# Performance work log

Measured on AMD Instinct MI355X. Metric: run time of the kernel, lower is better.

The kernel has to match this reference:

```python
import jax, jax.numpy as jnp
import numpy as np

EMBED = 1024
HEADS = 16
HDIM = EMBED // HEADS
B, S = 4, 2048
NEG = -1e20


def setup_inputs() -> dict:
    key = jax.random.key(0)
    ks = jax.random.split(key, 9)
    query = jax.random.normal(ks[0], (B, S, EMBED), dtype=jnp.float32)
    key_t = jax.random.normal(ks[1], (B, S, EMBED), dtype=jnp.float32)
    value = jax.random.normal(ks[2], (B, S, EMBED), dtype=jnp.float32)
    mask = jax.random.randint(ks[3], (1, 1, S, S), 0, 2, dtype=jnp.int32)
    padding = jax.random.randint(ks[4], (B, 1, 1, S), 0, 2, dtype=jnp.int32)
    sc = 1.0 / np.sqrt(EMBED)
    Wq = jax.random.normal(ks[5], (EMBED, EMBED), dtype=jnp.float32) * sc
    Wk = jax.random.normal(ks[6], (EMBED, EMBED), dtype=jnp.float32) * sc
    Wv = jax.random.normal(ks[7], (EMBED, EMBED), dtype=jnp.float32) * sc
    Wo = jax.random.normal(ks[8], (EMBED, EMBED), dtype=jnp.float32) * sc
    return {"query": query, "key": key_t, "value": value, "mask": mask,
            "padding": padding, "Wq": Wq, "Wk": Wk, "Wv": Wv, "Wo": Wo}


def reference(query, key, value, mask, padding, Wq, Wk, Wv, Wo):
    b, q_len, _ = query.shape
    k_len = key.shape[1]
    # projections (nn.Linear: x @ W^T), split into heads
    qs = (query @ Wq.T).reshape(b, q_len, HEADS, HDIM)
    ks = (key @ Wk.T).reshape(b, k_len, HEADS, HDIM)
    vs = (value @ Wv.T).reshape(b, k_len, HEADS, HDIM)
    scale = EMBED ** 0.25
    qs = qs / scale
    ks = ks / scale
    # [b, h, q, k] scores
    dot = jnp.einsum('bkhd,bqhd->bhqk', ks, qs)
    dot = jnp.where(mask == 0, NEG, dot)
    dot = jnp.where(padding == 0, NEG, dot)
    attn = jax.nn.softmax(dot, axis=-1)
    alpha = jnp.einsum('bhqk,bkhd->bqhd', attn, vs)
    out = alpha.reshape(b, q_len, EMBED) @ Wo.T
    return out
```

## Files before the change

kernel.cpp:

```cpp
#include <hip/hip_runtime.h>
#include <stdint.h>

#define B_  4
#define S_  2048
#define E_  1024
#define H_  16
#define D_  64

typedef __bf16 bf16;
typedef __bf16 bf16x4 __attribute__((ext_vector_type(4)));
typedef __bf16 bf16x8 __attribute__((ext_vector_type(8)));
typedef float  f32x4 __attribute__((ext_vector_type(4)));
typedef float  f32x16 __attribute__((ext_vector_type(16)));
typedef uint32_t u32x4 __attribute__((ext_vector_type(4)));

__device__ __forceinline__ f32x4 mfma16(bf16x8 a, bf16x8 b, f32x4 c) {
  return __builtin_amdgcn_mfma_f32_16x16x32_bf16(a, b, c, 0, 0, 0);
}
__device__ __forceinline__ f32x16 mfma32(bf16x8 a, bf16x8 b, f32x16 c) {
  return __builtin_amdgcn_mfma_f32_32x32x16_bf16(a, b, c, 0, 0, 0);
}

__device__ __forceinline__ int sw(int row, int idx) { return idx ^ ((row & 7) << 3); }

__device__ __forceinline__ void gl_lds16(const void* g, void* l) {
  __builtin_amdgcn_global_load_lds(
      (const __attribute__((address_space(1))) void*)g,
      (__attribute__((address_space(3))) void*)l, 16, 0, 0);
}

__device__ __forceinline__ uint32_t cvtpk(float lo, float hi) {
  uint32_t r;
  asm("v_cvt_pk_bf16_f32 %0, %1, %2" : "=v"(r) : "v"(lo), "v"(hi));
  return r;
}
__device__ __forceinline__ void plswap(uint32_t& a, uint32_t& b) {
  asm("v_permlane32_swap_b32 %0, %1" : "+v"(a), "+v"(b));
}

__global__ void pack_mask_kernel(const int* __restrict__ mask, uint32_t* __restrict__ mbits) {
  int idx = blockIdx.x * 256 + threadIdx.x;
  int q = idx >> 6, w = idx & 63;
  const int* p = mask + q * S_ + w * 32;
  uint32_t bits = 0;
#pragma unroll
  for (int j = 0; j < 32; j += 4) {
    int4 v = *(const int4*)(p + j);
    bits |= (v.x != 0 ? 1u : 0u) << (j + 0);
    bits |= (v.y != 0 ? 1u : 0u) << (j + 1);
    bits |= (v.z != 0 ? 1u : 0u) << (j + 2);
    bits |= (v.w != 0 ? 1u : 0u) << (j + 3);
  }
  mbits[idx] = bits;
}

__global__ void pack_pad_kernel(const int* __restrict__ pad, uint32_t* __restrict__ pbits) {
  int idx = threadIdx.x;
  int b = idx >> 6, w = idx & 63;
  const int* p = pad + b * S_ + w * 32;
  uint32_t bits = 0;
#pragma unroll
  for (int j = 0; j < 32; j += 4) {
    int4 v = *(const int4*)(p + j);
    bits |= (v.x != 0 ? 1u : 0u) << (j + 0);
    bits |= (v.y != 0 ? 1u : 0u) << (j + 1);
    bits |= (v.z != 0 ? 1u : 0u) << (j + 2);
    bits |= (v.w != 0 ? 1u : 0u) << (j + 3);
  }
  pbits[idx] = bits;
}

__global__ __launch_bounds__(256)
void cvt_act(const float* __restrict__ q, const float* __restrict__ k,
             const float* __restrict__ v, bf16* __restrict__ out) {
  const float* src = blockIdx.z == 0 ? q : (blockIdx.z == 1 ? k : v);
  size_t i = ((size_t)blockIdx.x * 256 + threadIdx.x) * 8;
  float4 a = *(const float4*)(src + i);
  float4 b = *(const float4*)(src + i + 4);
  bf16x8 o;
  o[0] = (bf16)a.x; o[1] = (bf16)a.y; o[2] = (bf16)a.z; o[3] = (bf16)a.w;
  o[4] = (bf16)b.x; o[5] = (bf16)b.y; o[6] = (bf16)b.z; o[7] = (bf16)b.w;
  *(bf16x8*)(out + (size_t)blockIdx.z * (8192ull * 1024ull) + i) = o;
}

__global__ __launch_bounds__(256)
void cvt_w(const float* __restrict__ w0, const float* __restrict__ w1,
           const float* __restrict__ w2, const float* __restrict__ w3,
           bf16* __restrict__ out, float sq, float sk) {
  int z = blockIdx.z;
  const float* src = z == 0 ? w0 : (z == 1 ? w1 : (z == 2 ? w2 : w3));
  float s = (z == 0) ? sq : ((z == 1) ? sk : 1.0f);
  size_t i = ((size_t)blockIdx.x * 256 + threadIdx.x) * 8;
  float4 a = *(const float4*)(src + i);
  float4 b = *(const float4*)(src + i + 4);
  bf16x8 o;
  o[0] = (bf16)(a.x * s); o[1] = (bf16)(a.y * s); o[2] = (bf16)(a.z * s); o[3] = (bf16)(a.w * s);
  o[4] = (bf16)(b.x * s); o[5] = (bf16)(b.y * s); o[6] = (bf16)(b.z * s); o[7] = (bf16)(b.w * s);
  *(bf16x8*)(out + (size_t)z * (1024ull * 1024ull) + i) = o;
}

struct GA { const bf16* A; const bf16* W; void* O; };

template<bool OUT_F32>
__global__ __launch_bounds__(256, 2)
void gemm_bf(GA g0, GA g1, GA g2) {
  GA g = (blockIdx.z == 0) ? g0 : ((blockIdx.z == 1) ? g1 : g2);
  const int tid = threadIdx.x;
  const int l = tid & 63, wv = tid >> 6;
  const int lg = l >> 4, lr = l & 15;
  const int wr = wv >> 1, wc = wv & 1;
  const int brow = blockIdx.x * 128, bcol = blockIdx.y * 128;
  const int sr = l >> 3, sc8 = l & 7;

  __shared__ bf16 As[128 * 64];
  __shared__ bf16 Bs[128 * 64];

  f32x4 acc[4][4] = {};

  const bf16* Ab = g.A + (size_t)(brow + wv * 32 + sr) * E_ + (size_t)(sc8 ^ sr) * 8;
  const bf16* Bb = g.W + (size_t)(bcol + wv * 32 + sr) * E_ + (size_t)(sc8 ^ sr) * 8;
  bf16* la = As + (wv * 32) * 64;
  bf16* lb = Bs + (wv * 32) * 64;

  for (int kt = 0; kt < E_ / 64; ++kt) {
    __syncthreads();
    const bf16* a = Ab + kt * 64;
    const bf16* b = Bb + kt * 64;
#pragma unroll
    for (int i = 0; i < 4; ++i) {
      gl_lds16(a + (size_t)i * 8 * E_, la + i * 8 * 64);
      gl_lds16(b + (size_t)i * 8 * E_, lb + i * 8 * 64);
    }
    __syncthreads();
#pragma unroll
    for (int kk = 0; kk < 2; ++kk) {
      bf16x8 af[4], bfr[4];
#pragma unroll
      for (int ms = 0; ms < 4; ++ms) {
        int row = wr * 64 + ms * 16 + lr;
        af[ms] = *(const bf16x8*)&As[sw(row, row * 64 + kk * 32 + lg * 8)];
      }
#pragma unroll
      for (int ns = 0; ns < 4; ++ns) {
        int row = wc * 64 + ns * 16 + lr;
        bfr[ns] = *(const bf16x8*)&Bs[sw(row, row * 64 + kk * 32 + lg * 8)];
      }
#pragma unroll
      for (int ms = 0; ms < 4; ++ms)
#pragma unroll
        for (int ns = 0; ns < 4; ++ns)
          acc[ms][ns] = mfma16(af[ms], bfr[ns], acc[ms][ns]);
    }
  }
#pragma unroll
  for (int ms = 0; ms < 4; ++ms) {
#pragma unroll
    for (int ns = 0; ns < 4; ++ns) {
#pragma unroll
      for (int r = 0; r < 4; ++r) {
        int row = brow + wr * 64 + ms * 16 + lg * 4 + r;
        int col = bcol + wc * 64 + ns * 16 + lr;
        if constexpr (OUT_F32) ((float*)g.O)[(size_t)row * E_ + col] = acc[ms][ns][r];
        else                   ((bf16*)g.O)[(size_t)row * E_ + col] = (bf16)acc[ms][ns][r];
      }
    }
  }
}

__global__ __launch_bounds__(256, 2)
void transpose_v(const bf16* __restrict__ V, bf16* __restrict__ Vt) {
  int bh = blockIdx.y; int b = bh >> 4, h = bh & 15;
  int s0 = blockIdx.x * 64;
  int tid = threadIdx.x;
  __shared__ bf16 t[64][72];
  int rb = tid >> 3, seg = tid & 7;
#pragma unroll
  for (int i = 0; i < 2; ++i) {
    int row = rb + 32 * i;
    bf16x8 v = *(const bf16x8*)(V + (size_t)(b * S_ + s0 + row) * E_ + h * 64 + seg * 8);
#pragma unroll
    for (int j = 0; j < 8; ++j) t[row][seg * 8 + j] = v[j];
  }
  __syncthreads();
#pragma unroll
  for (int i = 0; i < 2; ++i) {
    int d = rb + 32 * i;
    bf16x8 v;
#pragma unroll
    for (int j = 0; j < 8; ++j) v[j] = t[seg * 8 + j][d];
    *(bf16x8*)(Vt + ((size_t)bh * 64 + d) * S_ + s0 + seg * 8) = v;
  }
}

__global__ __launch_bounds__(256, 2)
void attn_kernel(const bf16* __restrict__ Q, const bf16* __restrict__ K,
                 const bf16* __restrict__ Vt, const uint32_t* __restrict__ mbits,
                 const uint32_t* __restrict__ pbits, bf16* __restrict__ alpha) {
  const int raw = blockIdx.x;
  const int xcd = raw & 7, slot = raw >> 3;
  const int bh = xcd * 8 + (slot >> 3), qblk = slot & 7;
  const int b = bh >> 4, h = bh & 15;
  const int tid = threadIdx.x, wv = tid >> 6, l = tid & 63;
  const int ln = l & 31, hi = l >> 5;
  const int qw = qblk * 256 + wv * 64;
  const int sr = l >> 3, sc8 = l & 7;
  const int g = (ln & 7) ^ (ln >> 3);

  __shared__ bf16 Ks[2][64 * 64];
  __shared__ bf16 Vs[2][64 * 64];

  bf16x8 qreg[2][4];
#pragma unroll
  for (int qt = 0; qt < 2; ++qt)
#pragma unroll
    for (int dc = 0; dc < 4; ++dc)
      qreg[qt][dc] = *(const bf16x8*)(Q + (size_t)(b * S_ + qw + qt * 32 + ln) * E_
                                        + h * 64 + dc * 16 + hi * 8);

  bf16x8 ones;
#pragma unroll
  for (int j = 0; j < 8; ++j) ones[j] = (bf16)1.0f;

  f32x16 o[2][2] = {};
  f32x16 lacc[2] = {};

  const bf16* Kb = K + (size_t)b * S_ * E_ + (size_t)h * 64;
  const bf16* Vb = Vt + (size_t)bh * 64 * S_;

  auto stage = [&](int buf, int kt) {
#pragma unroll
    for (int op = 0; op < 2; ++op) {
      int rb = wv * 16 + op * 8;
      int cK = (sc8 ^ sr ^ ((rb >> 3) & 7)) * 8;
      gl_lds16(Kb + (size_t)(kt * 64 + rb + sr) * E_ + cK, Ks[buf] + rb * 64);
      gl_lds16(Vb + (size_t)(rb + sr) * S_ + kt * 64 + cK, Vs[buf] + rb * 64);
    }
  };

  stage(0, 0);
  __syncthreads();

  for (int kt = 0; kt < S_ / 64; ++kt) {
    const int cur = kt & 1;
    if (kt + 1 < S_ / 64) stage(cur ^ 1, kt + 1);

    f32x16 sc[2][2] = {};
    __builtin_amdgcn_s_setprio(1);
#pragma unroll
    for (int ct = 0; ct < 2; ++ct) {
#pragma unroll
      for (int dc = 0; dc < 4; ++dc) {
        int row = ct * 32 + ln;
        int c = (dc * 2 + hi) ^ g ^ (ct * 4);
        bf16x8 kf = *(const bf16x8*)&Ks[cur][row * 64 + c * 8];
#pragma unroll
        for (int qt = 0; qt < 2; ++qt)
          sc[ct][qt] = mfma32(kf, qreg[qt][dc], sc[ct][qt]);
      }
    }
    __builtin_amdgcn_s_setprio(0);

    uint32_t pw0 = pbits[b * 64 + kt * 2], pw1 = pbits[b * 64 + kt * 2 + 1];
    uint32_t mq[2][2];
#pragma unroll
    for (int qt = 0; qt < 2; ++qt) {
      uint2 mv = *(const uint2*)(mbits + (size_t)(qw + qt * 32 + ln) * 64 + kt * 2);
      mq[qt][0] = (mv.x & pw0) >> (hi * 4);
      mq[qt][1] = (mv.y & pw1) >> (hi * 4);
    }

    uint32_t up[2][16];
#pragma unroll
    for (int qt = 0; qt < 2; ++qt) {
#pragma unroll
      for (int ct = 0; ct < 2; ++ct) {
        float p[16];
#pragma unroll
        for (int r = 0; r < 16; ++r) {
          const int rel = (r & 3) + 8 * (r >> 2);
          float pe = __builtin_amdgcn_exp2f(sc[ct][qt][r]);
          uint32_t keep = (uint32_t)__builtin_amdgcn_sbfe(mq[qt][ct], rel, 1);
          p[r] = __builtin_bit_cast(float, __builtin_bit_cast(uint32_t, pe) & keep);
        }
#pragma unroll
        for (int j = 0; j < 8; ++j)
          up[qt][ct * 8 + j] = cvtpk(p[2 * j], p[2 * j + 1]);
      }
    }

#pragma unroll
    for (int kc = 0; kc < 4; ++kc) {
      const int ct = kc >> 1, base = ct * 8 + (kc & 1) * 4;
      bf16x8 pf[2];
#pragma unroll
      for (int qt = 0; qt < 2; ++qt) {
        plswap(up[qt][base + 0], up[qt][base + 2]);
        plswap(up[qt][base + 1], up[qt][base + 3]);
        u32x4 w = {up[qt][base + 0], up[qt][base + 1], up[qt][base + 2], up[qt][base + 3]};
        pf[qt] = __builtin_bit_cast(bf16x8, w);
      }
      __builtin_amdgcn_s_setprio(1);
#pragma unroll
      for (int dt = 0; dt < 2; ++dt) {
        int row = dt * 32 + ln;
        int c = (kc * 2 + hi) ^ g ^ (dt * 4);
        bf16x8 vf = *(const bf16x8*)&Vs[cur][row * 64 + c * 8];
#pragma unroll
        for (int qt = 0; qt < 2; ++qt)
          o[dt][qt] = mfma32(vf, pf[qt], o[dt][qt]);
      }
#pragma unroll
      for (int qt = 0; qt < 2; ++qt)
        lacc[qt] = mfma32(ones, pf[qt], lacc[qt]);
      __builtin_amdgcn_s_setprio(0);
    }
    __syncthreads();
  }

#pragma unroll
  for (int qt = 0; qt < 2; ++qt) {
    float inv = 1.0f / lacc[qt][0];
    size_t qoff = (size_t)(b * S_ + qw + qt * 32 + ln) * E_ + h * 64;
#pragma unroll
    for (int dt = 0; dt < 2; ++dt) {
#pragma unroll
      for (int rg = 0; rg < 4; ++rg) {
        bf16x4 ov;
#pragma unroll
        for (int j = 0; j < 4; ++j) ov[j] = (bf16)(o[dt][qt][rg * 4 + j] * inv);
        *(bf16x4*)(alpha + qoff + dt * 32 + rg * 8 + hi * 4) = ov;
      }
    }
  }
}

extern "C" void kernel_launch(void* const* d_in, const int* in_sizes, int n_in,
                              void* d_out, int out_size, void* d_ws, size_t ws_size,
                              hipStream_t stream) {
  const float* query = (const float*)d_in[0];
  const float* key_t = (const float*)d_in[1];
  const float* value = (const float*)d_in[2];
  const int*   mask  = (const int*)d_in[3];
  const int*   pad   = (const int*)d_in[4];
  const float* Wq    = (const float*)d_in[5];
  const float* Wk    = (const float*)d_in[6];
  const float* Wv    = (const float*)d_in[7];
  const float* Wo    = (const float*)d_in[8];

  char* ws = (char*)d_ws;
  bf16* Abuf = (bf16*)ws;
  bf16* Vt    = (bf16*)ws;
  bf16* alpha = (bf16*)(ws + ((size_t)16 << 20));
  bf16* Wb   = (bf16*)(ws + ((size_t)48 << 20));
  bf16* QKV  = (bf16*)(ws + ((size_t)56 << 20));
  uint32_t* mbits = (uint32_t*)(ws + ((size_t)104 << 20));
  uint32_t* pbits = mbits + (size_t)S_ * 64;

  const size_t AM = 8192ull * 1024ull;
  const size_t WM = 1024ull * 1024ull;

  pack_mask_kernel<<<512, 256, 0, stream>>>(mask, mbits);
  pack_pad_kernel<<<1, 256, 0, stream>>>(pad, pbits);

  cvt_act<<<dim3(4096, 1, 3), 256, 0, stream>>>(query, key_t, value, Abuf);
  const float qscale = 0.17677669529663687f;
  const float log2e  = 1.4426950408889634f;
  cvt_w<<<dim3(512, 1, 4), 256, 0, stream>>>(Wq, Wk, Wv, Wo, Wb, qscale * log2e, qscale);

  GA gq{Abuf,          Wb,          QKV};
  GA gk{Abuf + AM,     Wb + WM,     QKV + AM};
  GA gv{Abuf + 2 * AM, Wb + 2 * WM, QKV + 2 * AM};
  gemm_bf<false><<<dim3(64, 8, 3), 256, 0, stream>>>(gq, gk, gv);

  transpose_v<<<dim3(32, 64), 256, 0, stream>>>(QKV + 2 * AM, Vt);

  attn_kernel<<<512, 256, 0, stream>>>(QKV, QKV + AM, Vt, mbits, pbits, alpha);

  GA go{alpha, Wb + 3 * WM, d_out};
  gemm_bf<true><<<dim3(64, 8, 1), 256, 0, stream>>>(go, go, go);
}
```

Measured before the change: 237.2 us.

## Fuse V transpose into projection GEMM epilogue and halve attention query tile

The V-projection GEMM now writes its output already transposed to the per-head [bh][d][s] layout through an LDS staging tile, so the separate transpose_v kernel and its extra global round trip go away. Separately, the attention kernel now handles 32 query rows per wave instead of 64, doubling the grid to 1024 blocks and raising launch bounds to 4 blocks per CU. This trades less K/V reuse per block (more LDS staging traffic per query) for higher occupancy and better latency hiding.

```diff
diff --git a/kernel.cpp b/kernel.cpp
--- a/kernel.cpp
+++ b/kernel.cpp
@@ -112,8 +112,9 @@
   const int brow = blockIdx.x * 128, bcol = blockIdx.y * 128;
   const int sr = l >> 3, sc8 = l & 7;
 
-  __shared__ bf16 As[128 * 64];
-  __shared__ bf16 Bs[128 * 64];
+  __shared__ bf16 Ls[2][128 * 64];
+  bf16* As = Ls[0];
+  bf16* Bs = Ls[1];
 
   f32x4 acc[4][4] = {};
 
@@ -152,6 +153,37 @@
           acc[ms][ns] = mfma16(af[ms], bfr[ns], acc[ms][ns]);
     }
   }
+
+  if (!OUT_F32 && blockIdx.z == 2) {
+    bf16* T = &Ls[0][0];
+    __syncthreads();
+#pragma unroll
+    for (int ms = 0; ms < 4; ++ms) {
+#pragma unroll
+      for (int ns = 0; ns < 4; ++ns) {
+        int col = wc * 64 + ns * 16 + lr;
+        int rowb = wr * 64 + ms * 16 + lg * 4;
+        bf16x4 hv;
+#pragma unroll
+        for (int r = 0; r < 4; ++r) hv[r] = (bf16)acc[ms][ns][r];
+        *(bf16x4*)&T[col * 128 + (rowb ^ ((col & 7) << 3))] = hv;
+      }
+    }
+    __syncthreads();
+    int chunk = tid & 15, dl0 = tid >> 4;
+#pragma unroll
+    for (int pass = 0; pass < 8; ++pass) {
+      int dl = pass * 16 + dl0;
+      bf16x8 v = *(const bf16x8*)&T[dl * 128 + ((chunk * 8) ^ ((dl & 7) << 3))];
+      int colg = bcol + dl;
+      int bh2 = (brow >> 11) * 16 + (colg >> 6);
+      int d = colg & 63;
+      int s0 = (brow & 2047) + chunk * 8;
+      *(bf16x8*)((bf16*)g.O + ((size_t)bh2 * 64 + d) * (size_t)S_ + s0) = v;
+    }
+    return;
+  }
+
 #pragma unroll
   for (int ms = 0; ms < 4; ++ms) {
 #pragma unroll
@@ -167,62 +199,34 @@
   }
 }
 
-__global__ __launch_bounds__(256, 2)
-void transpose_v(const bf16* __restrict__ V, bf16* __restrict__ Vt) {
-  int bh = blockIdx.y; int b = bh >> 4, h = bh & 15;
-  int s0 = blockIdx.x * 64;
-  int tid = threadIdx.x;
-  __shared__ bf16 t[64][72];
-  int rb = tid >> 3, seg = tid & 7;
-#pragma unroll
-  for (int i = 0; i < 2; ++i) {
-    int row = rb + 32 * i;
-    bf16x8 v = *(const bf16x8*)(V + (size_t)(b * S_ + s0 + row) * E_ + h * 64 + seg * 8);
-#pragma unroll
-    for (int j = 0; j < 8; ++j) t[row][seg * 8 + j] = v[j];
-  }
-  __syncthreads();
-#pragma unroll
-  for (int i = 0; i < 2; ++i) {
-    int d = rb + 32 * i;
-    bf16x8 v;
-#pragma unroll
-    for (int j = 0; j < 8; ++j) v[j] = t[seg * 8 + j][d];
-    *(bf16x8*)(Vt + ((size_t)bh * 64 + d) * S_ + s0 + seg * 8) = v;
-  }
-}
-
-__global__ __launch_bounds__(256, 2)
+__global__ __launch_bounds__(256, 4)
 void attn_kernel(const bf16* __restrict__ Q, const bf16* __restrict__ K,
                  const bf16* __restrict__ Vt, const uint32_t* __restrict__ mbits,
                  const uint32_t* __restrict__ pbits, bf16* __restrict__ alpha) {
   const int raw = blockIdx.x;
   const int xcd = raw & 7, slot = raw >> 3;
-  const int bh = xcd * 8 + (slot >> 3), qblk = slot & 7;
+  const int bh = xcd * 8 + (slot >> 4), qblk = slot & 15;
   const int b = bh >> 4, h = bh & 15;
   const int tid = threadIdx.x, wv = tid >> 6, l = tid & 63;
   const int ln = l & 31, hi = l >> 5;
-  const int qw = qblk * 256 + wv * 64;
+  const int qw = qblk * 128 + wv * 32;
   const int sr = l >> 3, sc8 = l & 7;
   const int g = (ln & 7) ^ (ln >> 3);
 
   __shared__ bf16 Ks[2][64 * 64];
   __shared__ bf16 Vs[2][64 * 64];
 
-  bf16x8 qreg[2][4];
-#pragma unroll
-  for (int qt = 0; qt < 2; ++qt)
-#pragma unroll
-    for (int dc = 0; dc < 4; ++dc)
-      qreg[qt][dc] = *(const bf16x8*)(Q + (size_t)(b * S_ + qw + qt * 32 + ln) * E_
-                                        + h * 64 + dc * 16 + hi * 8);
+  bf16x8 qreg[4];
+#pragma unroll
+  for (int dc = 0; dc < 4; ++dc)
+    qreg[dc] = *(const bf16x8*)(Q + (size_t)(b * S_ + qw + ln) * E_ + h * 64 + dc * 16 + hi * 8);
 
   bf16x8 ones;
 #pragma unroll
   for (int j = 0; j < 8; ++j) ones[j] = (bf16)1.0f;
 
-  f32x16 o[2][2] = {};
-  f32x16 lacc[2] = {};
+  f32x16 o[2] = {};
+  f32x16 lacc = {};
 
   const bf16* Kb = K + (size_t)b * S_ * E_ + (size_t)h * 64;
   const bf16* Vb = Vt + (size_t)bh * 64 * S_;
@@ -244,7 +248,7 @@
     const int cur = kt & 1;
     if (kt + 1 < S_ / 64) stage(cur ^ 1, kt + 1);
 
-    f32x16 sc[2][2] = {};
+    f32x16 sc[2] = {};
     __builtin_amdgcn_s_setprio(1);
 #pragma unroll
     for (int ct = 0; ct < 2; ++ct) {
@@ -253,83 +257,64 @@
         int row = ct * 32 + ln;
         int c = (dc * 2 + hi) ^ g ^ (ct * 4);
         bf16x8 kf = *(const bf16x8*)&Ks[cur][row * 64 + c * 8];
-#pragma unroll
-        for (int qt = 0; qt < 2; ++qt)
-          sc[ct][qt] = mfma32(kf, qreg[qt][dc], sc[ct][qt]);
+        sc[ct] = mfma32(kf, qreg[dc], sc[ct]);
       }
     }
     __builtin_amdgcn_s_setprio(0);
 
     uint32_t pw0 = pbits[b * 64 + kt * 2], pw1 = pbits[b * 64 + kt * 2 + 1];
-    uint32_t mq[2][2];
-#pragma unroll
-    for (int qt = 0; qt < 2; ++qt) {
-      uint2 mv = *(const uint2*)(mbits + (size_t)(qw + qt * 32 + ln) * 64 + kt * 2);
-      mq[qt][0] = (mv.x & pw0) >> (hi * 4);
-      mq[qt][1] = (mv.y & pw1) >> (hi * 4);
-    }
-
-    uint32_t up[2][16];
-#pragma unroll
-    for (int qt = 0; qt < 2; ++qt) {
-#pragma unroll
-      for (int ct = 0; ct < 2; ++ct) {
-        float p[16];
-#pragma unroll
-        for (int r = 0; r < 16; ++r) {
-          const int rel = (r & 3) + 8 * (r >> 2);
-          float pe = __builtin_amdgcn_exp2f(sc[ct][qt][r]);
-          uint32_t keep = (uint32_t)__builtin_amdgcn_sbfe(mq[qt][ct], rel, 1);
-          p[r] = __builtin_bit_cast(float, __builtin_bit_cast(uint32_t, pe) & keep);
-        }
-#pragma unroll
-        for (int j = 0; j < 8; ++j)
-          up[qt][ct * 8 + j] = cvtpk(p[2 * j], p[2 * j + 1]);
-      }
+    uint2 mv = *(const uint2*)(mbits + (size_t)(qw + ln) * 64 + kt * 2);
+    uint32_t mq[2];
+    mq[0] = (mv.x & pw0) >> (hi * 4);
+    mq[1] = (mv.y & pw1) >> (hi * 4);
+
+    uint32_t up[16];
+#pragma unroll
+    for (int ct = 0; ct < 2; ++ct) {
+      float p[16];
+#pragma unroll
+      for (int r = 0; r < 16; ++r) {
+        const int rel = (r & 3) + 8 * (r >> 2);
+        float pe = __builtin_amdgcn_exp2f(sc[ct][r]);
+        uint32_t keep = (uint32_t)__builtin_amdgcn_sbfe(mq[ct], rel, 1);
+        p[r] = __builtin_bit_cast(float, __builtin_bit_cast(uint32_t, pe) & keep);
+      }
+#pragma unroll
+      for (int j = 0; j < 8; ++j)
+        up[ct * 8 + j] = cvtpk(p[2 * j], p[2 * j + 1]);
     }
 
 #pragma unroll
     for (int kc = 0; kc < 4; ++kc) {
       const int ct = kc >> 1, base = ct * 8 + (kc & 1) * 4;
-      bf16x8 pf[2];
-#pragma unroll
-      for (int qt = 0; qt < 2; ++qt) {
-        plswap(up[qt][base + 0], up[qt][base + 2]);
-        plswap(up[qt][base + 1], up[qt][base + 3]);
-        u32x4 w = {up[qt][base + 0], up[qt][base + 1], up[qt][base + 2], up[qt][base + 3]};
-        pf[qt] = __builtin_bit_cast(bf16x8, w);
-      }
+      plswap(up[base + 0], up[base + 2]);
+      plswap(up[base + 1], up[base + 3]);
+      u32x4 w = {up[base + 0], up[base + 1], up[base + 2], up[base + 3]};
+      bf16x8 pf = __builtin_bit_cast(bf16x8, w);
       __builtin_amdgcn_s_setprio(1);
 #pragma unroll
       for (int dt = 0; dt < 2; ++dt) {
         int row = dt * 32 + ln;
         int c = (kc * 2 + hi) ^ g ^ (dt * 4);
         bf16x8 vf = *(const bf16x8*)&Vs[cur][row * 64 + c * 8];
-#pragma unroll
-        for (int qt = 0; qt < 2; ++qt)
-          o[dt][qt] = mfma32(vf, pf[qt], o[dt][qt]);
-      }
-#pragma unroll
-      for (int qt = 0; qt < 2; ++qt)
-        lacc[qt] = mfma32(ones, pf[qt], lacc[qt]);
+        o[dt] = mfma32(vf, pf, o[dt]);
+      }
+      lacc = mfma32(ones, pf, lacc);
       __builtin_amdgcn_s_setprio(0);
     }
     __syncthreads();
   }
 
-#pragma unroll
-  for (int qt = 0; qt < 2; ++qt) {
-    float inv = 1.0f / lacc[qt][0];
-    size_t qoff = (size_t)(b * S_ + qw + qt * 32 + ln) * E_ + h * 64;
-#pragma unroll
-    for (int dt = 0; dt < 2; ++dt) {
-#pragma unroll
-      for (int rg = 0; rg < 4; ++rg) {
-        bf16x4 ov;
-#pragma unroll
-        for (int j = 0; j < 4; ++j) ov[j] = (bf16)(o[dt][qt][rg * 4 + j] * inv);
-        *(bf16x4*)(alpha + qoff + dt * 32 + rg * 8 + hi * 4) = ov;
-      }
+  float inv = 1.0f / lacc[0];
+  size_t qoff = (size_t)(b * S_ + qw + ln) * E_ + h * 64;
+#pragma unroll
+  for (int dt = 0; dt < 2; ++dt) {
+#pragma unroll
+    for (int rg = 0; rg < 4; ++rg) {
+      bf16x4 ov;
+#pragma unroll
+      for (int j = 0; j < 4; ++j) ov[j] = (bf16)(o[dt][rg * 4 + j] * inv);
+      *(bf16x4*)(alpha + qoff + dt * 32 + rg * 8 + hi * 4) = ov;
     }
   }
 }
@@ -348,16 +333,16 @@
   const float* Wo    = (const float*)d_in[8];
 
   char* ws = (char*)d_ws;
-  bf16* Abuf = (bf16*)ws;
-  bf16* Vt    = (bf16*)ws;
+  bf16* Abuf  = (bf16*)ws;
   bf16* alpha = (bf16*)(ws + ((size_t)16 << 20));
-  bf16* Wb   = (bf16*)(ws + ((size_t)48 << 20));
-  bf16* QKV  = (bf16*)(ws + ((size_t)56 << 20));
+  bf16* Wb    = (bf16*)(ws + ((size_t)48 << 20));
+  bf16* QKV   = (bf16*)(ws + ((size_t)56 << 20));
   uint32_t* mbits = (uint32_t*)(ws + ((size_t)104 << 20));
   uint32_t* pbits = mbits + (size_t)S_ * 64;
 
   const size_t AM = 8192ull * 1024ull;
   const size_t WM = 1024ull * 1024ull;
+  bf16* Vt = QKV + 2 * AM;
 
   pack_mask_kernel<<<512, 256, 0, stream>>>(mask, mbits);
   pack_pad_kernel<<<1, 256, 0, stream>>>(pad, pbits);
@@ -369,12 +354,10 @@
 
   GA gq{Abuf,          Wb,          QKV};
   GA gk{Abuf + AM,     Wb + WM,     QKV + AM};
-  GA gv{Abuf + 2 * AM, Wb + 2 * WM, QKV + 2 * AM};
+  GA gv{Abuf + 2 * AM, Wb + 2 * WM, Vt};
   gemm_bf<false><<<dim3(64, 8, 3), 256, 0, stream>>>(gq, gk, gv);
 
-  transpose_v<<<dim3(32, 64), 256, 0, stream>>>(QKV + 2 * AM, Vt);
-
-  attn_kernel<<<512, 256, 0, stream>>>(QKV, QKV + AM, Vt, mbits, pbits, alpha);
+  attn_kernel<<<1024, 256, 0, stream>>>(QKV, QKV + AM, Vt, mbits, pbits, alpha);
 
   GA go{alpha, Wb + 3 * WM, d_out};
   gemm_bf<true><<<dim3(64, 8, 1), 256, 0, stream>>>(go, go, go);
```

Result: faster. 222.9 us (-6.0%).
